# Optimization experiments

Measured on AMD Instinct MI355X. Metric: run time of the kernel, lower is better.

## Reference

```python
import jax, jax.numpy as jnp
import numpy as np

N_NODES = 100000
N_EDGES = 3200000
F_IN = 256
H = 256
L = 256
BN_EPS = 1e-5


def gcn_conv(x, src, dst, deg_inv_sqrt, W, b):
    # x: [N, Fin]; src/dst: [E+N] (self-loops appended); returns [N, Fout]
    h = x @ W  # dense transform first (Fout may be < Fin)
    norm = deg_inv_sqrt[src] * deg_inv_sqrt[dst]  # [E+N]
    msg = h[src] * norm[:, None]                  # gather
    out = jax.ops.segment_sum(msg, dst, num_segments=N_NODES)  # scatter-add
    return out + b


def batch_norm(x, gamma, beta):
    # BatchNorm1d in training mode: per-feature mean/var over the node dim
    mean = jnp.mean(x, axis=0)
    var = jnp.var(x, axis=0)
    return (x - mean) * jax.lax.rsqrt(var + BN_EPS) * gamma + beta


def setup_inputs() -> dict:
    key = jax.random.key(0)
    ks = jax.random.split(key, 8)
    x = jax.random.normal(ks[0], (N_NODES, F_IN), dtype=jnp.float32)
    edge_index = jax.random.randint(ks[1], (2, N_EDGES), 0, N_NODES, dtype=jnp.int64)
    # glorot-ish init for weights
    W1 = jax.random.normal(ks[2], (F_IN, H), dtype=jnp.float32) * (1.0 / np.sqrt(F_IN))
    b1 = jnp.zeros((H,), dtype=jnp.float32)
    W_mu = jax.random.normal(ks[3], (H, L), dtype=jnp.float32) * (1.0 / np.sqrt(H))
    b_mu = jnp.zeros((L,), dtype=jnp.float32)
    W_ls = jax.random.normal(ks[4], (H, L), dtype=jnp.float32) * (1.0 / np.sqrt(H))
    b_ls = jnp.zeros((L,), dtype=jnp.float32)
    gamma = jnp.ones((H,), dtype=jnp.float32)
    beta = jnp.zeros((H,), dtype=jnp.float32)
    return {"x": x, "edge_index": edge_index, "W1": W1, "b1": b1,
            "W_mu": W_mu, "b_mu": b_mu, "W_ls": W_ls, "b_ls": b_ls,
            "gamma": gamma, "beta": beta}


def reference(x, edge_index, W1, b1, W_mu, b_mu, W_ls, b_ls, gamma, beta):
    # Add self-loops once (shared across the three GCNConv layers)
    loop = jnp.arange(N_NODES, dtype=edge_index.dtype)
    src = jnp.concatenate([edge_index[0], loop])
    dst = jnp.concatenate([edge_index[1], loop])
    deg = jax.ops.segment_sum(jnp.ones_like(dst, dtype=jnp.float32), dst,
                              num_segments=N_NODES)
    deg_inv_sqrt = jnp.where(deg > 0, jax.lax.rsqrt(jnp.maximum(deg, 1.0)), 0.0)

    h = gcn_conv(x, src, dst, deg_inv_sqrt, W1, b1)
    h = jax.nn.relu(batch_norm(h, gamma, beta))
    mu = gcn_conv(h, src, dst, deg_inv_sqrt, W_mu, b_mu)
    logstd = gcn_conv(h, src, dst, deg_inv_sqrt, W_ls, b_ls)
    return (mu, logstd)
```

## Files before the change

### kernel.cpp

```cpp
#include <hip/hip_runtime.h>
#include <hip/hip_bf16.h>

#define FEAT 256
#define NPB 512
#define NPB_SHIFT 9
#define MAXBINS 256
#define BIN_CHUNK 8192

typedef __attribute__((ext_vector_type(8))) short bf16x8;
typedef __attribute__((ext_vector_type(8))) ushort u16x8;
typedef __attribute__((ext_vector_type(4))) float f32x4;

__device__ __forceinline__ float bf2f(ushort h) {
    union { unsigned u; float f; } v; v.u = ((unsigned)h) << 16; return v.f;
}
__device__ __forceinline__ ushort f2bf(float f) {
    union { float f; unsigned u; } v; v.f = f;
    unsigned u = v.u;
    return (ushort)((u + 0x7FFFu + ((u >> 16) & 1u)) >> 16);
}


__global__ void k_deginit(int* __restrict__ deg, int n) {
    int i = blockIdx.x * blockDim.x + threadIdx.x;
    if (i < n) deg[i] = 1;
}

__global__ void k_deg(const int* __restrict__ ei, int E, int* __restrict__ deg) {
    int e = blockIdx.x * blockDim.x + threadIdx.x;
    int stride = gridDim.x * blockDim.x;
    for (; e < E; e += stride) {
        int d = ei[E + e];
        atomicAdd(&deg[d], 1);
    }
}

__global__ __launch_bounds__(256) void k_part(const int* __restrict__ deg,
                                              float* __restrict__ dis,
                                              int* __restrict__ bsum, int n) {
    int i = blockIdx.x * 256 + threadIdx.x;
    int v = (i < n) ? deg[i] : 0;
    if (i < n) dis[i] = rsqrtf((float)v);
    __shared__ int ws_[4];
    int s = v;
    #pragma unroll
    for (int o = 1; o < 64; o <<= 1) s += __shfl_xor(s, o, 64);
    if ((threadIdx.x & 63) == 0) ws_[threadIdx.x >> 6] = s;
    __syncthreads();
    if (threadIdx.x == 0) bsum[blockIdx.x] = ws_[0] + ws_[1] + ws_[2] + ws_[3];
}

__global__ __launch_bounds__(512) void k_scanb(const int* __restrict__ bsum,
                                               int* __restrict__ bpre,
                                               int* __restrict__ offs_n, int nb) {
    __shared__ int s[512];
    int t = threadIdx.x;
    int v = (t < nb) ? bsum[t] : 0;
    s[t] = v;
    __syncthreads();
    for (int d = 1; d < 512; d <<= 1) {
        int x = (t >= d) ? s[t - d] : 0;
        __syncthreads();
        s[t] += x;
        __syncthreads();
    }
    if (t < nb) bpre[t] = s[t] - v;
    if (t == nb - 1) offs_n[0] = s[t];
}

__global__ __launch_bounds__(256) void k_offsets(const int* __restrict__ deg,
                                                 const int* __restrict__ bpre,
                                                 int* __restrict__ offs,
                                                 int* __restrict__ bincur, int n) {
    __shared__ int s[256];
    int i = blockIdx.x * 256 + threadIdx.x;
    int t = threadIdx.x;
    int v = (i < n) ? deg[i] : 0;
    s[t] = v;
    __syncthreads();
    for (int d = 1; d < 256; d <<= 1) {
        int x = (t >= d) ? s[t - d] : 0;
        __syncthreads();
        s[t] += x;
        __syncthreads();
    }
    if (i < n) {
        int o = bpre[blockIdx.x] + s[t] - v;
        offs[i] = o;
        if ((i & (NPB - 1)) == 0) bincur[i >> NPB_SHIFT] = o;
    }
}


__global__ __launch_bounds__(256) void k_bin(const int* __restrict__ ei, int E, int N,
                                             int* __restrict__ bincur,
                                             int2* __restrict__ binbuf, int nbins) {
    __shared__ int hist[MAXBINS];
    __shared__ int base[MAXBINS];
    int t = threadIdx.x;
    int T = E + N;
    int start = blockIdx.x * BIN_CHUNK;
    int end = min(start + BIN_CHUNK, T);
    for (int b = t; b < nbins; b += 256) hist[b] = 0;
    __syncthreads();
    for (int idx = start + t; idx < end; idx += 256) {
        int d = (idx < E) ? ei[E + idx] : idx - E;
        atomicAdd(&hist[d >> NPB_SHIFT], 1);
    }
    __syncthreads();
    for (int b = t; b < nbins; b += 256) {
        int c = hist[b];
        base[b] = c ? atomicAdd(&bincur[b], c) : 0;
        hist[b] = 0;
    }
    __syncthreads();
    for (int idx = start + t; idx < end; idx += 256) {
        int s, d;
        if (idx < E) { s = ei[idx]; d = ei[E + idx]; }
        else         { s = idx - E; d = idx - E; }
        int b = d >> NPB_SHIFT;
        int local = atomicAdd(&hist[b], 1);
        binbuf[base[b] + local] = make_int2(s, d);
    }
}


__global__ __launch_bounds__(256) void k_csr(const int2* __restrict__ binbuf,
                                             const int* __restrict__ offs,
                                             int* __restrict__ csr, int N) {
    __shared__ int soffs[NPB + 1];
    __shared__ int cur[NPB];
    int b = blockIdx.x;
    int node0 = b * NPB;
    int nn = min(NPB, N - node0);
    int t = threadIdx.x;
    for (int i = t; i <= nn; i += 256) soffs[i] = offs[node0 + i];
    for (int i = t; i < nn; i += 256) cur[i] = 0;
    __syncthreads();
    int rbeg = soffs[0], rend = soffs[nn];
    for (int idx = rbeg + t; idx < rend; idx += 256) {
        int2 e = binbuf[idx];
        int ld = e.y - node0;
        int c = atomicAdd(&cur[ld], 1);
        csr[soffs[ld] + c] = e.x;
    }
}


__global__ __launch_bounds__(256) void k_cvt(const float* __restrict__ x,
                                             ushort* __restrict__ y,
                                             const float* __restrict__ dis, int n4) {
    int i = blockIdx.x * blockDim.x + threadIdx.x;
    int stride = gridDim.x * blockDim.x;
    for (; i < n4; i += stride) {
        float d = dis[i >> 6];
        float4 v = ((const float4*)x)[i];
        ushort4 o;
        o.x = f2bf(v.x * d); o.y = f2bf(v.y * d);
        o.z = f2bf(v.z * d); o.w = f2bf(v.w * d);
        ((ushort4*)y)[i] = o;
    }
}


__global__ void k_wprep(const float* __restrict__ W1, const float* __restrict__ Wmu,
                        const float* __restrict__ Wls, const float* __restrict__ bmu,
                        const float* __restrict__ bls,
                        ushort* __restrict__ Wt1, ushort* __restrict__ Wtc,
                        float* __restrict__ biasc, float* __restrict__ bnacc) {
    int i = blockIdx.x * 256 + threadIdx.x;
    int m = i >> 16;
    int j = i & 65535;
    int n = j >> 8, k = j & 255;
    const float* W = (m == 0) ? W1 : (m == 1) ? Wmu : Wls;
    ushort v = f2bf(W[k * 256 + n]);
    if (m == 0) Wt1[j] = v;
    else if (m == 1) Wtc[j] = v;
    else Wtc[65536 + j] = v;
    if (i < 512) { biasc[i] = (i < 256) ? bmu[i] : bls[i - 256]; bnacc[i] = 0.f; }
}


template <int NCOL, bool BF16OUT>
__global__ __launch_bounds__(512) void k_aggmm(const ushort* __restrict__ tab,
                                               const int* __restrict__ offs,
                                               const int* __restrict__ csr,
                                               const float* __restrict__ dis,
                                               const ushort* __restrict__ Bt,
                                               const float* __restrict__ bias,
                                               float* __restrict__ C0,
                                               float* __restrict__ C1,
                                               ushort* __restrict__ Cb,
                                               float* __restrict__ bnacc,
                                               int N) {
    __shared__ ushort At[128 * 256];
    __shared__ ushort Bs[128 * 64];
    int t = threadIdx.x;
    int wave = t >> 6;
    int lane = t & 63;
    int half = lane >> 5;
    int l32 = lane & 31;
    int rowbase = blockIdx.x * 128;

    for (int i = 0; i < 16; ++i) {
        int r = wave * 16 + i;
        int node = rowbase + r;
        float acc[8] = {};
        if (node < N) {
            int beg = offs[node], end = offs[node + 1];
            int k = beg;
            for (; k + 16 <= end; k += 16) {
                int s0 = csr[k + half];
                int s1 = csr[k + 2 + half];
                int s2 = csr[k + 4 + half];
                int s3 = csr[k + 6 + half];
                int s4 = csr[k + 8 + half];
                int s5 = csr[k + 10 + half];
                int s6 = csr[k + 12 + half];
                int s7 = csr[k + 14 + half];
                bf16x8 v0 = *(const bf16x8*)(tab + (size_t)s0 * FEAT + l32 * 8);
                bf16x8 v1 = *(const bf16x8*)(tab + (size_t)s1 * FEAT + l32 * 8);
                bf16x8 v2 = *(const bf16x8*)(tab + (size_t)s2 * FEAT + l32 * 8);
                bf16x8 v3 = *(const bf16x8*)(tab + (size_t)s3 * FEAT + l32 * 8);
                bf16x8 v4 = *(const bf16x8*)(tab + (size_t)s4 * FEAT + l32 * 8);
                bf16x8 v5 = *(const bf16x8*)(tab + (size_t)s5 * FEAT + l32 * 8);
                bf16x8 v6 = *(const bf16x8*)(tab + (size_t)s6 * FEAT + l32 * 8);
                bf16x8 v7 = *(const bf16x8*)(tab + (size_t)s7 * FEAT + l32 * 8);
                #pragma unroll
                for (int j = 0; j < 8; ++j) {
                    float t0 = bf2f((ushort)v0[j]) + bf2f((ushort)v1[j]);
                    float t1 = bf2f((ushort)v2[j]) + bf2f((ushort)v3[j]);
                    float t2 = bf2f((ushort)v4[j]) + bf2f((ushort)v5[j]);
                    float t3 = bf2f((ushort)v6[j]) + bf2f((ushort)v7[j]);
                    acc[j] += (t0 + t1) + (t2 + t3);
                }
            }
            for (; k + 2 <= end; k += 2) {
                int s = csr[k + half];
                bf16x8 v = *(const bf16x8*)(tab + (size_t)s * FEAT + l32 * 8);
                #pragma unroll
                for (int j = 0; j < 8; ++j) acc[j] += bf2f((ushort)v[j]);
            }
            if (k < end && half == 0) {
                int s = csr[k];
                bf16x8 v = *(const bf16x8*)(tab + (size_t)s * FEAT + l32 * 8);
                #pragma unroll
                for (int j = 0; j < 8; ++j) acc[j] += bf2f((ushort)v[j]);
            }
        }
        #pragma unroll
        for (int j = 0; j < 8; ++j) acc[j] += __shfl_xor(acc[j], 32, 64);
        if (half == 0) {
            float d = (node < N) ? dis[node] : 0.f;
            u16x8 o;
            #pragma unroll
            for (int j = 0; j < 8; ++j) o[j] = f2bf(acc[j] * d);
            int cs = (l32 & 24) | ((l32 & 7) ^ (r & 7));
            *(u16x8*)(At + r * 256 + cs * 8) = o;
        }
    }
    __syncthreads();

    constexpr int NH = NCOL / 128;
    int wm = wave >> 2, wn = wave & 3;
    int lo = lane & 15, g = lane >> 4;
    for (int nh = 0; nh < NH; ++nh) {
        f32x4 acc2[4][2] = {};
        for (int kt = 0; kt < 4; ++kt) {
            #pragma unroll
            for (int u = 0; u < 2; ++u) {
                int id = t + u * 512;
                int br = id >> 3, bc = id & 7;
                int lc = bc ^ (br & 7);
                bf16x8 bv = *(const bf16x8*)(Bt + (size_t)(nh * 128 + br) * 256 + kt * 64 + lc * 8);
                *(bf16x8*)(Bs + br * 64 + bc * 8) = bv;
            }
            __syncthreads();
            #pragma unroll
            for (int h = 0; h < 2; ++h) {
                bf16x8 af[4], bfr[2];
                #pragma unroll
                for (int m = 0; m < 4; ++m) {
                    int r = wm * 64 + m * 16 + lo;
                    af[m] = *(const bf16x8*)(At + r * 256 + (kt * 8 + ((h * 4 + g) ^ (r & 7))) * 8);
                }
                #pragma unroll
                for (int n = 0; n < 2; ++n) {
                    int r = wn * 32 + n * 16 + lo;
                    bfr[n] = *(const bf16x8*)(Bs + r * 64 + ((h * 4 + g) ^ (r & 7)) * 8);
                }
                #pragma unroll
                for (int m = 0; m < 4; ++m)
                    #pragma unroll
                    for (int n = 0; n < 2; ++n)
                        acc2[m][n] = __builtin_amdgcn_mfma_f32_16x16x32_bf16(
                            af[m], bfr[n], acc2[m][n], 0, 0, 0);
            }
            __syncthreads();
        }
        #pragma unroll
        for (int n = 0; n < 2; ++n) {
            int gc = nh * 128 + wn * 32 + n * 16 + lo;
            float bb = bias[gc];
            float s = 0.f, q = 0.f;
            #pragma unroll
            for (int m = 0; m < 4; ++m) {
                f32x4 v = acc2[m][n];
                #pragma unroll
                for (int r4 = 0; r4 < 4; ++r4) {
                    int grow = rowbase + wm * 64 + m * 16 + g * 4 + r4;
                    if (grow < N) {
                        float val = v[r4] + bb;
                        if (BF16OUT) {
                            Cb[(size_t)grow * 256 + gc] = f2bf(val);
                            s += val; q += val * val;
                        } else {
                            float* Cp = C0; int cc = gc;
                            if (gc >= 256) { Cp = C1; cc = gc - 256; }
                            __builtin_nontemporal_store(val, &Cp[(size_t)grow * 256 + cc]);
                        }
                    }
                }
            }
            if (BF16OUT) {
                s += __shfl_xor(s, 16, 64); s += __shfl_xor(s, 32, 64);
                q += __shfl_xor(q, 16, 64); q += __shfl_xor(q, 32, 64);
                if (g == 0) {
                    atomicAdd(&bnacc[gc], s);
                    atomicAdd(&bnacc[256 + gc], q);
                }
            }
        }
    }
}


__global__ __launch_bounds__(256) void k_bnapply(const ushort* __restrict__ h,
                                                 ushort* __restrict__ o,
                                                 const float* __restrict__ acc,
                                                 const float* __restrict__ gamma,
                                                 const float* __restrict__ beta,
                                                 const float* __restrict__ dis, int Nn) {
    int c4 = (threadIdx.x & 63) * 4;
    int rof = (int)threadIdx.x >> 6;
    float inv = 1.0f / (float)Nn;
    float g[4], b[4];
    #pragma unroll
    for (int j = 0; j < 4; ++j) {
        float mean = acc[c4 + j] * inv;
        float var = acc[FEAT + c4 + j] * inv - mean * mean;
        float rs = rsqrtf(var + 1e-5f);
        g[j] = gamma[c4 + j] * rs;
        b[j] = beta[c4 + j] - mean * g[j];
    }
    for (int r = blockIdx.x * 4 + rof; r < Nn; r += gridDim.x * 4) {
        float d = dis[r];
        ushort4 v = *(const ushort4*)(h + (size_t)r * FEAT + c4);
        float o0 = bf2f(v.x) * g[0] + b[0], o1 = bf2f(v.y) * g[1] + b[1];
        float o2 = bf2f(v.z) * g[2] + b[2], o3 = bf2f(v.w) * g[3] + b[3];
        ushort4 ov;
        ov.x = f2bf((o0 > 0.f ? o0 : 0.f) * d);
        ov.y = f2bf((o1 > 0.f ? o1 : 0.f) * d);
        ov.z = f2bf((o2 > 0.f ? o2 : 0.f) * d);
        ov.w = f2bf((o3 > 0.f ? o3 : 0.f) * d);
        *(ushort4*)(o + (size_t)r * FEAT + c4) = ov;
    }
}


extern "C" void kernel_launch(void* const* d_in, const int* in_sizes, int n_in,
                              void* d_out, int out_size, void* d_ws, size_t ws_size,
                              hipStream_t stream) {
    const float* x     = (const float*)d_in[0];
    const int*   ei    = (const int*)d_in[1];
    const float* W1    = (const float*)d_in[2];
    const float* b1    = (const float*)d_in[3];
    const float* Wmu   = (const float*)d_in[4];
    const float* bmu   = (const float*)d_in[5];
    const float* Wls   = (const float*)d_in[6];
    const float* bls   = (const float*)d_in[7];
    const float* gamma = (const float*)d_in[8];
    const float* beta  = (const float*)d_in[9];

    int N = in_sizes[0] / FEAT;
    int E = in_sizes[1] / 2;
    int nb = (N + 255) / 256;
    int nbins = (N + NPB - 1) / NPB;
    int T = E + N;

    float* out = (float*)d_out;
    float* mu  = out;
    float* ls  = out + (size_t)N * FEAT;
    ushort* xtab = (ushort*)mu;
    ushort* H1b  = (ushort*)ls;

    char* p = (char*)d_ws;
    auto alloc = [&](size_t bytes) -> void* {
        void* r = (void*)p;
        p += (bytes + 255) & ~(size_t)255;
        return r;
    };
    ushort* htab  = (ushort*)alloc((size_t)N * FEAT * 2);
    int2*   binbuf= (int2*)  alloc((size_t)T * 8);
    int*    csr   = (int*)   alloc((size_t)T * 4);
    int*    deg   = (int*)   alloc((size_t)N * 4);
    int*    offs  = (int*)   alloc((size_t)(N + 1) * 4);
    float*  dis   = (float*) alloc((size_t)N * 4);
    float*  bnacc = (float*) alloc(512 * 4);
    ushort* Wt1   = (ushort*)alloc(65536 * 2);
    ushort* Wtc   = (ushort*)alloc(131072 * 2);
    float*  biasc = (float*) alloc(512 * 4);
    int*    bsum  = (int*)   alloc((size_t)nb * 4);
    int*    bpre  = (int*)   alloc((size_t)nb * 4);
    int*    bincur= (int*)   alloc((size_t)nbins * 4);

    k_deginit<<<nb, 256, 0, stream>>>(deg, N);
    k_deg<<<4096, 256, 0, stream>>>(ei, E, deg);
    k_part<<<nb, 256, 0, stream>>>(deg, dis, bsum, N);
    k_scanb<<<1, 512, 0, stream>>>(bsum, bpre, offs + N, nb);
    k_offsets<<<nb, 256, 0, stream>>>(deg, bpre, offs, bincur, N);

    k_bin<<<(T + BIN_CHUNK - 1) / BIN_CHUNK, 256, 0, stream>>>(ei, E, N, bincur, binbuf, nbins);
    k_csr<<<nbins, 256, 0, stream>>>(binbuf, offs, csr, N);

    k_wprep<<<768, 256, 0, stream>>>(W1, Wmu, Wls, bmu, bls, Wt1, Wtc, biasc, bnacc);
    k_cvt<<<2048, 256, 0, stream>>>(x, xtab, dis, N * FEAT / 4);

    int gblocks = (N + 127) / 128;

    k_aggmm<256, true><<<gblocks, 512, 0, stream>>>(
        xtab, offs, csr, dis, Wt1, b1, nullptr, nullptr, H1b, bnacc, N);

    k_bnapply<<<2048, 256, 0, stream>>>(H1b, htab, bnacc, gamma, beta, dis, N);

    k_aggmm<512, false><<<gblocks, 512, 0, stream>>>(
        htab, offs, csr, dis, Wtc, biasc, mu, ls, nullptr, nullptr, N);
}
```

Baseline: 872.8 us.

## Bin edges into fixed-capacity buckets and shrink aggregation tiles to 64 rows

```diff
diff --git a/kernel.cpp b/kernel.cpp
--- a/kernel.cpp
+++ b/kernel.cpp
@@ -5,6 +5,7 @@
 #define NPB 512
 #define NPB_SHIFT 9
 #define MAXBINS 256
+#define CAP 20480
 #define BIN_CHUNK 8192
 
 typedef __attribute__((ext_vector_type(8))) short bf16x8;
@@ -18,77 +19,6 @@
     union { float f; unsigned u; } v; v.f = f;
     unsigned u = v.u;
     return (ushort)((u + 0x7FFFu + ((u >> 16) & 1u)) >> 16);
-}
-
-
-__global__ void k_deginit(int* __restrict__ deg, int n) {
-    int i = blockIdx.x * blockDim.x + threadIdx.x;
-    if (i < n) deg[i] = 1;
-}
-
-__global__ void k_deg(const int* __restrict__ ei, int E, int* __restrict__ deg) {
-    int e = blockIdx.x * blockDim.x + threadIdx.x;
-    int stride = gridDim.x * blockDim.x;
-    for (; e < E; e += stride) {
-        int d = ei[E + e];
-        atomicAdd(&deg[d], 1);
-    }
-}
-
-__global__ __launch_bounds__(256) void k_part(const int* __restrict__ deg,
-                                              float* __restrict__ dis,
-                                              int* __restrict__ bsum, int n) {
-    int i = blockIdx.x * 256 + threadIdx.x;
-    int v = (i < n) ? deg[i] : 0;
-    if (i < n) dis[i] = rsqrtf((float)v);
-    __shared__ int ws_[4];
-    int s = v;
-    #pragma unroll
-    for (int o = 1; o < 64; o <<= 1) s += __shfl_xor(s, o, 64);
-    if ((threadIdx.x & 63) == 0) ws_[threadIdx.x >> 6] = s;
-    __syncthreads();
-    if (threadIdx.x == 0) bsum[blockIdx.x] = ws_[0] + ws_[1] + ws_[2] + ws_[3];
-}
-
-__global__ __launch_bounds__(512) void k_scanb(const int* __restrict__ bsum,
-                                               int* __restrict__ bpre,
-                                               int* __restrict__ offs_n, int nb) {
-    __shared__ int s[512];
-    int t = threadIdx.x;
-    int v = (t < nb) ? bsum[t] : 0;
-    s[t] = v;
-    __syncthreads();
-    for (int d = 1; d < 512; d <<= 1) {
-        int x = (t >= d) ? s[t - d] : 0;
-        __syncthreads();
-        s[t] += x;
-        __syncthreads();
-    }
-    if (t < nb) bpre[t] = s[t] - v;
-    if (t == nb - 1) offs_n[0] = s[t];
-}
-
-__global__ __launch_bounds__(256) void k_offsets(const int* __restrict__ deg,
-                                                 const int* __restrict__ bpre,
-                                                 int* __restrict__ offs,
-                                                 int* __restrict__ bincur, int n) {
-    __shared__ int s[256];
-    int i = blockIdx.x * 256 + threadIdx.x;
-    int t = threadIdx.x;
-    int v = (i < n) ? deg[i] : 0;
-    s[t] = v;
-    __syncthreads();
-    for (int d = 1; d < 256; d <<= 1) {
-        int x = (t >= d) ? s[t - d] : 0;
-        __syncthreads();
-        s[t] += x;
-        __syncthreads();
-    }
-    if (i < n) {
-        int o = bpre[blockIdx.x] + s[t] - v;
-        offs[i] = o;
-        if ((i & (NPB - 1)) == 0) bincur[i >> NPB_SHIFT] = o;
-    }
 }
 
 
@@ -110,7 +40,7 @@
     __syncthreads();
     for (int b = t; b < nbins; b += 256) {
         int c = hist[b];
-        base[b] = c ? atomicAdd(&bincur[b], c) : 0;
+        base[b] = c ? (b * CAP + atomicAdd(&bincur[b], c)) : 0;
         hist[b] = 0;
     }
     __syncthreads();
@@ -125,7 +55,60 @@
 }
 
 
+__global__ __launch_bounds__(512) void k_scanb(const int* __restrict__ bsum,
+                                               int* __restrict__ bpre,
+                                               int* __restrict__ offs_n, int nb) {
+    __shared__ int s[512];
+    int t = threadIdx.x;
+    int v = (t < nb) ? bsum[t] : 0;
+    s[t] = v;
+    __syncthreads();
+    for (int d = 1; d < 512; d <<= 1) {
+        int x = (t >= d) ? s[t - d] : 0;
+        __syncthreads();
+        s[t] += x;
+        __syncthreads();
+    }
+    if (t < nb) bpre[t] = s[t] - v;
+    if (t == nb - 1) offs_n[0] = s[t];
+}
+
+
+__global__ __launch_bounds__(512) void k_histoffs(const int2* __restrict__ binbuf,
+                                                  const int* __restrict__ bincur,
+                                                  const int* __restrict__ bpre,
+                                                  int* __restrict__ offs,
+                                                  float* __restrict__ dis, int N) {
+    __shared__ int h[NPB];
+    int b = blockIdx.x;
+    int t = threadIdx.x;
+    int node0 = b * NPB;
+    int nn = min(NPB, N - node0);
+    h[t] = 0;
+    __syncthreads();
+    int cnt = bincur[b];
+    int base = b * CAP;
+    for (int i = t; i < cnt; i += 512) {
+        int d = binbuf[base + i].y;
+        atomicAdd(&h[d - node0], 1);
+    }
+    __syncthreads();
+    int v = h[t];
+    for (int d = 1; d < 512; d <<= 1) {
+        int x = (t >= d) ? h[t - d] : 0;
+        __syncthreads();
+        h[t] += x;
+        __syncthreads();
+    }
+    if (t < nn) {
+        offs[node0 + t] = bpre[b] + h[t] - v;
+        dis[node0 + t] = rsqrtf((float)v);
+    }
+}
+
+
 __global__ __launch_bounds__(256) void k_csr(const int2* __restrict__ binbuf,
+                                             const int* __restrict__ bincur,
                                              const int* __restrict__ offs,
                                              int* __restrict__ csr, int N) {
     __shared__ int soffs[NPB + 1];
@@ -137,9 +120,10 @@
     for (int i = t; i <= nn; i += 256) soffs[i] = offs[node0 + i];
     for (int i = t; i < nn; i += 256) cur[i] = 0;
     __syncthreads();
-    int rbeg = soffs[0], rend = soffs[nn];
-    for (int idx = rbeg + t; idx < rend; idx += 256) {
-        int2 e = binbuf[idx];
+    int cnt = bincur[b];
+    int base = b * CAP;
+    for (int idx = t; idx < cnt; idx += 256) {
+        int2 e = binbuf[base + idx];
         int ld = e.y - node0;
         int c = atomicAdd(&cur[ld], 1);
         csr[soffs[ld] + c] = e.x;
@@ -182,25 +166,25 @@
 
 
 template <int NCOL, bool BF16OUT>
-__global__ __launch_bounds__(512) void k_aggmm(const ushort* __restrict__ tab,
-                                               const int* __restrict__ offs,
-                                               const int* __restrict__ csr,
-                                               const float* __restrict__ dis,
-                                               const ushort* __restrict__ Bt,
-                                               const float* __restrict__ bias,
-                                               float* __restrict__ C0,
-                                               float* __restrict__ C1,
-                                               ushort* __restrict__ Cb,
-                                               float* __restrict__ bnacc,
-                                               int N) {
-    __shared__ ushort At[128 * 256];
-    __shared__ ushort Bs[128 * 64];
+__global__ __launch_bounds__(256, 4) void k_aggmm(const ushort* __restrict__ tab,
+                                                  const int* __restrict__ offs,
+                                                  const int* __restrict__ csr,
+                                                  const float* __restrict__ dis,
+                                                  const ushort* __restrict__ Bt,
+                                                  const float* __restrict__ bias,
+                                                  float* __restrict__ C0,
+                                                  float* __restrict__ C1,
+                                                  ushort* __restrict__ Cb,
+                                                  float* __restrict__ bnacc,
+                                                  int N) {
+    __shared__ ushort At[64 * 256];
+    __shared__ ushort Bs[64 * 64];
     int t = threadIdx.x;
     int wave = t >> 6;
     int lane = t & 63;
     int half = lane >> 5;
     int l32 = lane & 31;
-    int rowbase = blockIdx.x * 128;
+    int rowbase = blockIdx.x * 64;
 
     for (int i = 0; i < 16; ++i) {
         int r = wave * 16 + i;
@@ -261,36 +245,36 @@
     }
     __syncthreads();
 
-    constexpr int NH = NCOL / 128;
-    int wm = wave >> 2, wn = wave & 3;
+    constexpr int NH = NCOL / 64;
+    int wm = wave >> 1, wn = wave & 1;
     int lo = lane & 15, g = lane >> 4;
     for (int nh = 0; nh < NH; ++nh) {
-        f32x4 acc2[4][2] = {};
+        f32x4 acc2[2][2] = {};
         for (int kt = 0; kt < 4; ++kt) {
             #pragma unroll
             for (int u = 0; u < 2; ++u) {
-                int id = t + u * 512;
+                int id = t + u * 256;
                 int br = id >> 3, bc = id & 7;
                 int lc = bc ^ (br & 7);
-                bf16x8 bv = *(const bf16x8*)(Bt + (size_t)(nh * 128 + br) * 256 + kt * 64 + lc * 8);
+                bf16x8 bv = *(const bf16x8*)(Bt + (size_t)(nh * 64 + br) * 256 + kt * 64 + lc * 8);
                 *(bf16x8*)(Bs + br * 64 + bc * 8) = bv;
             }
             __syncthreads();
             #pragma unroll
             for (int h = 0; h < 2; ++h) {
-                bf16x8 af[4], bfr[2];
-                #pragma unroll
-                for (int m = 0; m < 4; ++m) {
-                    int r = wm * 64 + m * 16 + lo;
+                bf16x8 af[2], bfr[2];
+                #pragma unroll
+                for (int m = 0; m < 2; ++m) {
+                    int r = wm * 32 + m * 16 + lo;
                     af[m] = *(const bf16x8*)(At + r * 256 + (kt * 8 + ((h * 4 + g) ^ (r & 7))) * 8);
                 }
                 #pragma unroll
                 for (int n = 0; n < 2; ++n) {
-                    int r = wn * 32 + n * 16 + lo;
-                    bfr[n] = *(const bf16x8*)(Bs + r * 64 + ((h * 4 + g) ^ (r & 7)) * 8);
+                    int rb = wn * 32 + n * 16 + lo;
+                    bfr[n] = *(const bf16x8*)(Bs + rb * 64 + ((h * 4 + g) ^ (rb & 7)) * 8);
                 }
                 #pragma unroll
-                for (int m = 0; m < 4; ++m)
+                for (int m = 0; m < 2; ++m)
                     #pragma unroll
                     for (int n = 0; n < 2; ++n)
                         acc2[m][n] = __builtin_amdgcn_mfma_f32_16x16x32_bf16(
@@ -300,15 +284,15 @@
         }
         #pragma unroll
         for (int n = 0; n < 2; ++n) {
-            int gc = nh * 128 + wn * 32 + n * 16 + lo;
+            int gc = nh * 64 + wn * 32 + n * 16 + lo;
             float bb = bias[gc];
             float s = 0.f, q = 0.f;
             #pragma unroll
-            for (int m = 0; m < 4; ++m) {
+            for (int m = 0; m < 2; ++m) {
                 f32x4 v = acc2[m][n];
                 #pragma unroll
                 for (int r4 = 0; r4 < 4; ++r4) {
-                    int grow = rowbase + wm * 64 + m * 16 + g * 4 + r4;
+                    int grow = rowbase + wm * 32 + m * 16 + g * 4 + r4;
                     if (grow < N) {
                         float val = v[r4] + bb;
                         if (BF16OUT) {
@@ -384,7 +368,6 @@
 
     int N = in_sizes[0] / FEAT;
     int E = in_sizes[1] / 2;
-    int nb = (N + 255) / 256;
     int nbins = (N + NPB - 1) / NPB;
     int T = E + N;
 
@@ -401,38 +384,34 @@
         return r;
     };
     ushort* htab  = (ushort*)alloc((size_t)N * FEAT * 2);
-    int2*   binbuf= (int2*)  alloc((size_t)T * 8);
+    int2*   binbuf= (int2*)  alloc((size_t)nbins * CAP * 8);
     int*    csr   = (int*)   alloc((size_t)T * 4);
-    int*    deg   = (int*)   alloc((size_t)N * 4);
     int*    offs  = (int*)   alloc((size_t)(N + 1) * 4);
     float*  dis   = (float*) alloc((size_t)N * 4);
     float*  bnacc = (float*) alloc(512 * 4);
     ushort* Wt1   = (ushort*)alloc(65536 * 2);
     ushort* Wtc   = (ushort*)alloc(131072 * 2);
     float*  biasc = (float*) alloc(512 * 4);
-    int*    bsum  = (int*)   alloc((size_t)nb * 4);
-    int*    bpre  = (int*)   alloc((size_t)nb * 4);
+    int*    bpre  = (int*)   alloc((size_t)nbins * 4);
     int*    bincur= (int*)   alloc((size_t)nbins * 4);
 
-    k_deginit<<<nb, 256, 0, stream>>>(deg, N);
-    k_deg<<<4096, 256, 0, stream>>>(ei, E, deg);
-    k_part<<<nb, 256, 0, stream>>>(deg, dis, bsum, N);
-    k_scanb<<<1, 512, 0, stream>>>(bsum, bpre, offs + N, nb);
-    k_offsets<<<nb, 256, 0, stream>>>(deg, bpre, offs, bincur, N);
-
+    hipMemsetAsync(bincur, 0, (size_t)nbins * 4, stream);
     k_bin<<<(T + BIN_CHUNK - 1) / BIN_CHUNK, 256, 0, stream>>>(ei, E, N, bincur, binbuf, nbins);
-    k_csr<<<nbins, 256, 0, stream>>>(binbuf, offs, csr, N);
+
+    k_scanb<<<1, 512, 0, stream>>>(bincur, bpre, offs + N, nbins);
+    k_histoffs<<<nbins, 512, 0, stream>>>(binbuf, bincur, bpre, offs, dis, N);
+    k_csr<<<nbins, 256, 0, stream>>>(binbuf, bincur, offs, csr, N);
 
     k_wprep<<<768, 256, 0, stream>>>(W1, Wmu, Wls, bmu, bls, Wt1, Wtc, biasc, bnacc);
     k_cvt<<<2048, 256, 0, stream>>>(x, xtab, dis, N * FEAT / 4);
 
-    int gblocks = (N + 127) / 128;
-
-    k_aggmm<256, true><<<gblocks, 512, 0, stream>>>(
+    int gblocks = (N + 63) / 64;
+
+    k_aggmm<256, true><<<gblocks, 256, 0, stream>>>(
         xtab, offs, csr, dis, Wt1, b1, nullptr, nullptr, H1b, bnacc, N);
 
     k_bnapply<<<2048, 256, 0, stream>>>(H1b, htab, bnacc, gamma, beta, dis, N);
 
-    k_aggmm<512, false><<<gblocks, 512, 0, stream>>>(
+    k_aggmm<512, false><<<gblocks, 256, 0, stream>>>(
         htab, offs, csr, dis, Wtc, biasc, mu, ls, nullptr, nullptr, N);
 }
```

New measurement: 791.9 us. 1.1x faster.
